# Kernel tuning notes

Hardware: AMD Instinct MI355X
Metric: run time of the kernel (lower is better)

## Reference

```python
import jax, jax.numpy as jnp
import numpy as np

B, S, D, H = 4, 2048, 256, 8
HD = D // H
SCALE = float(np.sqrt(HD))  # temperature = head_dim ** 0.5


def setup_inputs() -> dict:
    key = jax.random.key(0)
    ks = jax.random.split(key, 12)
    w = lambda k, shape: jax.random.normal(k, shape, dtype=jnp.float32) * 0.05
    x = jax.random.normal(ks[0], (B, S, D), dtype=jnp.float32)
    adj = jax.random.randint(ks[1], (B, S, S), 0, 2, dtype=jnp.int32)
    return {
        "x": x,
        "adj": adj,
        "w_qkv": w(ks[2], (3 * D, D)),
        "b_qkv": jnp.zeros((3 * D,), jnp.float32),
        "ln_g": jnp.ones((D,), jnp.float32),
        "ln_b": jnp.zeros((D,), jnp.float32),
        "w_fc": w(ks[3], (D, D)),
        "b_fc": jnp.zeros((D,), jnp.float32),
        "w_z": w(ks[4], (D, D)),
        "b_z": jnp.full((D,), -2.0, jnp.float32),  # init_bias fills w_z bias with -2
        "u_z": w(ks[5], (D, D)),
        "w_r": w(ks[6], (D, D)),
        "u_r": w(ks[7], (D, D)),
        "w_g": w(ks[8], (D, D)),
        "u_g": w(ks[9], (D, D)),
    }


def reference(x, adj, w_qkv, b_qkv, ln_g, ln_b, w_fc, b_fc,
              w_z, b_z, u_z, w_r, u_r, w_g, u_g):
    residual = x
    # LayerNorm (eps=1e-5, torch default)
    mu = jnp.mean(x, axis=-1, keepdims=True)
    var = jnp.var(x, axis=-1, keepdims=True)
    xn = (x - mu) / jnp.sqrt(var + 1e-5) * ln_g + ln_b
    # fused QKV projection -> (B*H, S, 3*HD), batch-major over (b, h)
    qkv = xn @ w_qkv.T + b_qkv                       # [B,S,3D]
    qkv = qkv.reshape(B, S, H, 3 * HD).transpose(0, 2, 1, 3).reshape(B * H, S, 3 * HD)
    q, k, v = jnp.split(qkv, 3, axis=-1)
    # masked scaled dot-product attention (full NxN scores, as in original)
    attn = jnp.einsum('nqd,nkd->nqk', q, k) / SCALE  # [B*H,S,S]
    adj_r = jnp.repeat(adj, H, axis=0)               # batch-major, matches attn layout
    attn = jnp.where(adj_r == 0, -jnp.inf, attn)
    attn = jax.nn.softmax(attn, axis=-1)
    out = jnp.einsum('nqk,nkd->nqd', attn, v)        # [B*H,S,HD]
    # Faithful replication of torch's view(n_head, batch, ...) applied to
    # batch-major data (an ordering quirk in the original module).
    out = out.reshape(H, B, S, HD).transpose(1, 2, 0, 3).reshape(B, S, D)
    y = jax.nn.relu(out @ w_fc.T + b_fc)
    # GRU gate: x=residual, y=attention branch
    z = jax.nn.sigmoid(y @ w_z.T + b_z + residual @ u_z.T)
    r = jax.nn.sigmoid(y @ w_r.T + residual @ u_r.T)
    h_hat = jnp.tanh(y @ w_g.T + (r * residual) @ u_g.T)
    return (1.0 - z) * residual + z * h_hat
```

## Files before the change

### kernel.cpp

```cpp
#include <hip/hip_runtime.h>
#include <hip/hip_bf16.h>
#include <math.h>

#define B_  4
#define S_  2048
#define D_  256
#define H_  8
#define HD_ 32
#define QSCALE 0.25504175929589786f

typedef short  bf16x8 __attribute__((ext_vector_type(8)));
typedef float  f32x4  __attribute__((ext_vector_type(4)));
typedef unsigned short ushort_t;
typedef unsigned int   uint_t;

__device__ __forceinline__ ushort_t f2b(float f) {
    union { float f; unsigned u; } v; v.f = f;
    unsigned r = (v.u + 0x7FFFu + ((v.u >> 16) & 1u)) >> 16;
    return (ushort_t)r;
}
__device__ __forceinline__ float b2f(ushort_t s) {
    return __uint_as_float((uint_t)s << 16);
}

__device__ __forceinline__ float wave_sum(float v) {
#pragma unroll
    for (int o = 32; o > 0; o >>= 1) v += __shfl_down(v, o, 64);
    return v;
}
__device__ __forceinline__ float block_sum256(float v, float* scr) {
    v = wave_sum(v);
    int lane = threadIdx.x & 63, wid = threadIdx.x >> 6;
    if (lane == 0) scr[wid] = v;
    __syncthreads();
    float r = scr[0] + scr[1] + scr[2] + scr[3];
    __syncthreads();
    return r;
}

#define WQ_SZ 196608
#define WS_SZ 65536
#define NB_ADJ 8192
#define NB_WC  2560
#define NB_LN  8192
__global__ __launch_bounds__(256)
void prep_kernel(const int* __restrict__ adj, uint_t* __restrict__ bits,
                 const float* __restrict__ w0, const float* __restrict__ w1,
                 const float* __restrict__ w2, const float* __restrict__ w3,
                 const float* __restrict__ w4, const float* __restrict__ w5,
                 const float* __restrict__ w6, const float* __restrict__ w7,
                 ushort_t* __restrict__ wout,
                 const float* __restrict__ x, const float* __restrict__ g,
                 const float* __restrict__ bb, ushort_t* __restrict__ xn_b) {
    __shared__ float scr[4];
    int blk = blockIdx.x, tid = threadIdx.x;
    if (blk < NB_ADJ) {
        int lane = tid & 63;
#pragma unroll
        for (int gp = 0; gp < 8; ++gp) {
            size_t i = ((size_t)blk * 8 + gp) * 256 + tid;
            unsigned long long m = __ballot(adj[i] != 0);
            size_t wbase = (((size_t)blk * 8 + gp) * 256 + (tid & ~63)) >> 5;
            if (lane == 0)  bits[wbase]     = (uint_t)m;
            if (lane == 32) bits[wbase + 1] = (uint_t)(m >> 32);
        }
    } else if (blk < NB_ADJ + NB_WC) {
        int idx = (blk - NB_ADJ) * 256 + tid;
        const float* src; int o;
        if (idx < WQ_SZ) { src = w0; o = idx; }
        else {
            int j = idx - WQ_SZ, seg = j >> 16; o = j & (WS_SZ - 1);
            src = (seg == 0) ? w1 : (seg == 1) ? w2 : (seg == 2) ? w3 :
                  (seg == 3) ? w4 : (seg == 4) ? w5 : (seg == 5) ? w6 : w7;
        }
        int j  = o & 7;
        int l  = (o >> 3) & 15;
        int qd = (o >> 7) & 3;
        int ks = (o >> 9) & 7;
        int ct = o >> 12;
        wout[idx] = f2b(src[(ct * 16 + l) * 256 + ks * 32 + qd * 8 + j]);
    } else {
        size_t base = (size_t)(blk - NB_ADJ - NB_WC) * D_;
        float v  = x[base + tid];
        float mu = block_sum256(v, scr) * (1.0f / D_);
        float d  = v - mu;
        float var = block_sum256(d * d, scr) * (1.0f / D_);
        float rstd = rsqrtf(var + 1e-5f);
        xn_b[base + tid] = f2b(d * rstd * g[tid] + bb[tid]);
    }
}

__global__ __launch_bounds__(256)
void gemm_qkv(const ushort_t* __restrict__ A, const ushort_t* __restrict__ Wf,
              const float* __restrict__ bias, ushort_t* __restrict__ outb,
              ushort_t* __restrict__ vT) {
    __shared__ ushort_t Sa[64][264];
    int tid = threadIdx.x;
    int wave = tid >> 6, lane = tid & 63, l = lane & 15, quad = lane >> 4;
    int wm = wave >> 1, wn = wave & 1;
    int m0 = blockIdx.y * 64, n0 = blockIdx.x * 64;
    {
        int row = tid >> 2, c0 = (tid & 3) * 64;
        const ushort_t* ap = A + (size_t)(m0 + row) * 256 + c0;
#pragma unroll
        for (int j = 0; j < 8; ++j)
            *(uint4*)&Sa[row][c0 + 8 * j] = ((const uint4*)ap)[j];
    }
    __syncthreads();

    bf16x8 af[2][8];
#pragma unroll
    for (int mt = 0; mt < 2; ++mt)
#pragma unroll
        for (int ks = 0; ks < 8; ++ks)
            af[mt][ks] = *(const bf16x8*)&Sa[wm * 32 + mt * 16 + l][ks * 32 + quad * 8];

    f32x4 acc[2][2];
#pragma unroll
    for (int i = 0; i < 2; ++i)
#pragma unroll
        for (int j = 0; j < 2; ++j) acc[i][j] = (f32x4){0.f, 0.f, 0.f, 0.f};

#pragma unroll
    for (int nt = 0; nt < 2; ++nt) {
        int ct = (n0 >> 4) + wn * 2 + nt;
        bf16x8 wfr[8];
#pragma unroll
        for (int ks = 0; ks < 8; ++ks)
            wfr[ks] = *(const bf16x8*)(Wf + (((size_t)ct * 8 + ks) * 64 + lane) * 8);
#pragma unroll
        for (int ks = 0; ks < 8; ++ks) {
            acc[0][nt] = __builtin_amdgcn_mfma_f32_16x16x32_bf16(af[0][ks], wfr[ks], acc[0][nt], 0, 0, 0);
            acc[1][nt] = __builtin_amdgcn_mfma_f32_16x16x32_bf16(af[1][ks], wfr[ks], acc[1][nt], 0, 0, 0);
        }
    }

    __syncthreads();
    ushort_t* So = &Sa[0][0];
#pragma unroll
    for (int nt = 0; nt < 2; ++nt) {
        int col = wn * 32 + nt * 16 + l;
        int gcol = n0 + col;
        float bv = bias[gcol];
        float qs = ((gcol % 96) < 32) ? QSCALE : 1.0f;
#pragma unroll
        for (int mt = 0; mt < 2; ++mt)
#pragma unroll
            for (int r = 0; r < 4; ++r) {
                int row = wm * 32 + mt * 16 + quad * 4 + r;
                So[row * 72 + col] = f2b((acc[mt][nt][r] + bv) * qs);
            }
    }
    __syncthreads();
    {
        int row = tid >> 2, seg = tid & 3;
        uint4 v0 = *(uint4*)&So[row * 72 + seg * 16];
        uint4 v1 = *(uint4*)&So[row * 72 + seg * 16 + 8];
        ushort_t* op = outb + (size_t)(m0 + row) * 768 + n0 + seg * 16;
        ((uint4*)op)[0] = v0;
        ((uint4*)op)[1] = v1;
    }

    int vs = n0 % 96;
    if (vs != 0) {
        int vloc = (vs == 64) ? 0 : 32;
        int h  = (n0 + vloc) / 96;
        int b  = m0 >> 11;
        int s0 = m0 & (S_ - 1);
        ushort_t* vstage = &Sa[0][0] + 8192;
        {
            int c = tid & 31, seg = tid >> 5;
            ushort_t tmp[8];
#pragma unroll
            for (int i = 0; i < 8; ++i)
                tmp[i] = So[(seg * 8 + i) * 72 + vloc + c];
            uint_t u[4];
#pragma unroll
            for (int i = 0; i < 4; ++i)
                u[i] = (uint_t)tmp[2 * i] | ((uint_t)tmp[2 * i + 1] << 16);
            *(uint4*)&vstage[c * 72 + seg * 8] = make_uint4(u[0], u[1], u[2], u[3]);
        }
        __syncthreads();
        {
            int d = tid >> 3, tseg = tid & 7;
            uint4 v = *(uint4*)&vstage[d * 72 + tseg * 8];
            *(uint4*)&vT[((size_t)(b * 8 + h) * 32 + d) * S_ + s0 + tseg * 8] = v;
        }
    }
}

__global__ __launch_bounds__(256)
void fused_gate(const ushort_t* __restrict__ attn_b, const float* __restrict__ xf,
                const ushort_t* __restrict__ wfc, const ushort_t* __restrict__ wz,
                const ushort_t* __restrict__ uz, const ushort_t* __restrict__ wr,
                const ushort_t* __restrict__ ur, const ushort_t* __restrict__ wg,
                const ushort_t* __restrict__ ug, const float* __restrict__ bfc,
                const float* __restrict__ bz, float* __restrict__ out) {
    __shared__ ushort_t Sa[16][264];
    __shared__ ushort_t Sx[16][264];
    __shared__ ushort_t Sy[16][264];
    __shared__ ushort_t St[16][264];
    int tid = threadIdx.x;
    int wave = tid >> 6, lane = tid & 63, l = lane & 15, quad = lane >> 4;
    int m0 = blockIdx.x * 16;
    int colbase = wave * 64;

    {
        int row = tid >> 4, c0 = (tid & 15) * 16;
        const ushort_t* ap = attn_b + (size_t)(m0 + row) * 256 + c0;
        uint4 a0 = ((const uint4*)ap)[0];
        uint4 a1 = ((const uint4*)ap)[1];
        *(uint4*)&Sa[row][c0] = a0;
        *(uint4*)&Sa[row][c0 + 8] = a1;
        const float4* xp = (const float4*)(xf + (size_t)(m0 + row) * 256 + c0);
        float4 f0 = xp[0], f1 = xp[1], f2_ = xp[2], f3 = xp[3];
        union { __hip_bfloat162 h[4]; uint4 u; } p0, p1;
        p0.h[0] = __float22bfloat162_rn(make_float2(f0.x, f0.y));
        p0.h[1] = __float22bfloat162_rn(make_float2(f0.z, f0.w));
        p0.h[2] = __float22bfloat162_rn(make_float2(f1.x, f1.y));
        p0.h[3] = __float22bfloat162_rn(make_float2(f1.z, f1.w));
        p1.h[0] = __float22bfloat162_rn(make_float2(f2_.x, f2_.y));
        p1.h[1] = __float22bfloat162_rn(make_float2(f2_.z, f2_.w));
        p1.h[2] = __float22bfloat162_rn(make_float2(f3.x, f3.y));
        p1.h[3] = __float22bfloat162_rn(make_float2(f3.z, f3.w));
        *(uint4*)&Sx[row][c0]     = p0.u;
        *(uint4*)&Sx[row][c0 + 8] = p1.u;
    }
    __syncthreads();

    {
        bf16x8 af[8];
#pragma unroll
        for (int ks = 0; ks < 8; ++ks)
            af[ks] = *(const bf16x8*)&Sa[l][ks * 32 + quad * 8];
        f32x4 ya[4];
#pragma unroll
        for (int nt = 0; nt < 4; ++nt) ya[nt] = (f32x4){0.f, 0.f, 0.f, 0.f};
#pragma unroll
        for (int nt = 0; nt < 4; ++nt) {
            size_t fb = ((size_t)(wave * 4 + nt) * 8) * 512 + lane * 8;
#pragma unroll
            for (int ks = 0; ks < 8; ++ks) {
                bf16x8 wfr = *(const bf16x8*)(wfc + fb + ks * 512);
                ya[nt] = __builtin_amdgcn_mfma_f32_16x16x32_bf16(af[ks], wfr, ya[nt], 0, 0, 0);
            }
        }
#pragma unroll
        for (int nt = 0; nt < 4; ++nt) {
            int col = colbase + nt * 16 + l;
            float bv = bfc[col];
#pragma unroll
            for (int r = 0; r < 4; ++r)
                Sy[quad * 4 + r][col] = f2b(fmaxf(ya[nt][r] + bv, 0.0f));
        }
    }
    __syncthreads();

    f32x4 az[4], ar[4], ag[4];
#pragma unroll
    for (int nt = 0; nt < 4; ++nt) {
        az[nt] = (f32x4){0.f, 0.f, 0.f, 0.f};
        ar[nt] = (f32x4){0.f, 0.f, 0.f, 0.f};
        ag[nt] = (f32x4){0.f, 0.f, 0.f, 0.f};
    }
#pragma unroll
    for (int nt = 0; nt < 4; ++nt) {
        size_t fb = ((size_t)(wave * 4 + nt) * 8) * 512 + lane * 8;
#pragma unroll
        for (int ks = 0; ks < 8; ++ks) {
            bf16x8 fy = *(const bf16x8*)&Sy[l][ks * 32 + quad * 8];
            bf16x8 fx = *(const bf16x8*)&Sx[l][ks * 32 + quad * 8];
            bf16x8 fz  = *(const bf16x8*)(wz + fb + ks * 512);
            bf16x8 fuz = *(const bf16x8*)(uz + fb + ks * 512);
            bf16x8 fr  = *(const bf16x8*)(wr + fb + ks * 512);
            bf16x8 fur = *(const bf16x8*)(ur + fb + ks * 512);
            bf16x8 fg  = *(const bf16x8*)(wg + fb + ks * 512);
            az[nt] = __builtin_amdgcn_mfma_f32_16x16x32_bf16(fy, fz,  az[nt], 0, 0, 0);
            az[nt] = __builtin_amdgcn_mfma_f32_16x16x32_bf16(fx, fuz, az[nt], 0, 0, 0);
            ar[nt] = __builtin_amdgcn_mfma_f32_16x16x32_bf16(fy, fr,  ar[nt], 0, 0, 0);
            ar[nt] = __builtin_amdgcn_mfma_f32_16x16x32_bf16(fx, fur, ar[nt], 0, 0, 0);
            ag[nt] = __builtin_amdgcn_mfma_f32_16x16x32_bf16(fy, fg,  ag[nt], 0, 0, 0);
        }
    }
#pragma unroll
    for (int nt = 0; nt < 4; ++nt) {
        int col = colbase + nt * 16 + l;
        float bzv = bz[col];
#pragma unroll
        for (int r = 0; r < 4; ++r) {
            int row = quad * 4 + r;
            az[nt][r] = 1.0f / (1.0f + __expf(-(az[nt][r] + bzv)));
            float rr  = 1.0f / (1.0f + __expf(-ar[nt][r]));
            St[row][col] = f2b(rr * b2f(Sx[row][col]));
        }
    }
    __syncthreads();

    f32x4 fcc[4];
#pragma unroll
    for (int nt = 0; nt < 4; ++nt) fcc[nt] = (f32x4){0.f, 0.f, 0.f, 0.f};
#pragma unroll
    for (int nt = 0; nt < 4; ++nt) {
        size_t fb = ((size_t)(wave * 4 + nt) * 8) * 512 + lane * 8;
#pragma unroll
        for (int ks = 0; ks < 8; ++ks) {
            bf16x8 ft = *(const bf16x8*)&St[l][ks * 32 + quad * 8];
            bf16x8 fu = *(const bf16x8*)(ug + fb + ks * 512);
            fcc[nt] = __builtin_amdgcn_mfma_f32_16x16x32_bf16(ft, fu, fcc[nt], 0, 0, 0);
        }
    }
#pragma unroll
    for (int nt = 0; nt < 4; ++nt) {
        int col = colbase + nt * 16 + l;
#pragma unroll
        for (int r = 0; r < 4; ++r) {
            int row = quad * 4 + r;
            float v = ag[nt][r] + fcc[nt][r];
            float e = __expf(2.0f * v);
            float h = 1.0f - 2.0f / (e + 1.0f);
            float zz = az[nt][r];
            size_t idx = (size_t)(m0 + row) * 256 + col;
            out[idx] = (1.0f - zz) * xf[idx] + zz * h;
        }
    }
}

__global__ __launch_bounds__(256)
void attn_kernel(const ushort_t* __restrict__ qkvb, const ushort_t* __restrict__ vT,
                 const uint_t* __restrict__ abits, ushort_t* __restrict__ attn_b) {
    __shared__ ushort_t Ks[2][64][40];
    __shared__ ushort_t Vt[2][32][72];
    __shared__ ushort_t Ps[64][72];

    int tid = threadIdx.x;
    int wave = tid >> 6, lane = tid & 63, l = lane & 15, quad = lane >> 4;

    int lid = blockIdx.y * 32 + blockIdx.x;
    int L   = (lid & 7) * 128 + (lid >> 3);
    int q0  = (L & 31) * 64;
    int n   = L >> 5;
    int b = n >> 3, h = n & 7;
    int bp = n & 3, hp = n >> 2;

    const ushort_t* base = qkvb + (size_t)b * S_ * 768 + h * 96;
    int myq = wave * 16 + l;
    int qsh = quad * 4;

    bf16x8 qf = *(const bf16x8*)(base + (size_t)(q0 + myq) * 768 + quad * 8);

    bf16x8 ones;
#pragma unroll
    for (int i = 0; i < 8; ++i) ones[i] = (short)0x3F80;

    f32x4 oacc[2], aones;
    oacc[0] = (f32x4){0.f, 0.f, 0.f, 0.f};
    oacc[1] = (f32x4){0.f, 0.f, 0.f, 0.f};
    aones   = (f32x4){0.f, 0.f, 0.f, 0.f};

    int skey = tid >> 2, spart = tid & 3;
    int kcol = (spart * 8) ^ (((skey >> 3) & 1) << 3);
    int vd = tid >> 3, vk = (tid & 7) * 8;
    const ushort_t* vptr = vT + ((size_t)n * 32 + vd) * S_ + vk;
    const uint_t* aptr = abits + ((size_t)b * S_ + q0 + myq) * 64;

    uint2 aw = *(const uint2*)(aptr);
    {
        uint4 k0v = *(const uint4*)(base + (size_t)skey * 768 + 32 + spart * 8);
        uint4 v0v = *(const uint4*)(vptr);
        *(uint4*)&Ks[0][skey][kcol] = k0v;
        *(uint4*)&Vt[0][vd][vk] = v0v;
    }
    uint4 kv = *(const uint4*)(base + (size_t)(64 + skey) * 768 + 32 + spart * 8);
    uint4 vv = *(const uint4*)(vptr + 64);
    __syncthreads();

    for (int k0 = 0; k0 < S_; k0 += 64) {
        int cur = (k0 >> 6) & 1;
        bool more = (k0 + 64 < S_);
        uint2 awn;
        if (more) {
            *(uint4*)&Ks[cur ^ 1][skey][kcol] = kv;
            *(uint4*)&Vt[cur ^ 1][vd][vk] = vv;
            awn = *(const uint2*)(aptr + ((k0 + 64) >> 5));
            if (k0 + 128 < S_) {
                kv = *(const uint4*)(base + (size_t)(k0 + 128 + skey) * 768 + 32 + spart * 8);
                vv = *(const uint4*)(vptr + k0 + 128);
            }
        }
        uint_t aw0 = aw.x, aw1 = aw.y;

#pragma unroll
        for (int t4 = 0; t4 < 4; ++t4) {
            bf16x8 kf = *(const bf16x8*)&Ks[cur][t4 * 16 + l][(quad * 8) ^ ((l >> 3) << 3)];
            f32x4 z = (f32x4){0.f, 0.f, 0.f, 0.f};
            f32x4 sc = __builtin_amdgcn_mfma_f32_16x16x32_bf16(kf, qf, z, 0, 0, 0);
            uint_t w = (t4 & 2) ? aw1 : aw0;
            uint_t idx = (w >> ((t4 & 1) * 16 + qsh)) & 15u;
            union { __hip_bfloat162 b2[2]; uint2 u2; } pk;
            pk.b2[0] = __float22bfloat162_rn(make_float2(exp2f(sc[0]), exp2f(sc[1])));
            pk.b2[1] = __float22bfloat162_rn(make_float2(exp2f(sc[2]), exp2f(sc[3])));
            pk.u2.x &= ((idx & 1u) ? 0xFFFFu : 0u) | ((idx & 2u) ? 0xFFFF0000u : 0u);
            pk.u2.y &= ((idx & 4u) ? 0xFFFFu : 0u) | ((idx & 8u) ? 0xFFFF0000u : 0u);
            *(uint2*)&Ps[myq][t4 * 16 + qsh] = pk.u2;
        }

        __builtin_amdgcn_s_setprio(1);
#pragma unroll
        for (int ks = 0; ks < 2; ++ks) {
            bf16x8 pf = *(const bf16x8*)&Ps[myq][ks * 32 + quad * 8];
            aones = __builtin_amdgcn_mfma_f32_16x16x32_bf16(ones, pf, aones, 0, 0, 0);
#pragma unroll
            for (int mt = 0; mt < 2; ++mt) {
                bf16x8 vf = *(const bf16x8*)&Vt[cur][mt * 16 + l][ks * 32 + quad * 8];
                oacc[mt] = __builtin_amdgcn_mfma_f32_16x16x32_bf16(vf, pf, oacc[mt], 0, 0, 0);
            }
        }
        __builtin_amdgcn_s_setprio(0);

        if (more) aw = awn;
        __syncthreads();
    }

    float linv = 1.0f / aones[0];

    ushort_t* Ost = &Ks[0][0][0];
#pragma unroll
    for (int mt = 0; mt < 2; ++mt)
#pragma unroll
        for (int r = 0; r < 4; ++r)
            Ost[myq * 40 + mt * 16 + quad * 4 + r] = f2b(oacc[mt][r] * linv);
    __syncthreads();
    {
        int q = tid >> 2, part = tid & 3;
        uint4 v = *(uint4*)&Ost[q * 40 + part * 8];
        *(uint4*)&attn_b[((size_t)(bp * S_ + q0 + q)) * 256 + hp * 32 + part * 8] = v;
    }
}

extern "C" void kernel_launch(void* const* d_in, const int* in_sizes, int n_in,
                              void* d_out, int out_size, void* d_ws, size_t ws_size,
                              hipStream_t stream) {
    const float* x     = (const float*)d_in[0];
    const int*   adj   = (const int*)d_in[1];
    const float* w_qkv = (const float*)d_in[2];
    const float* b_qkv = (const float*)d_in[3];
    const float* ln_g  = (const float*)d_in[4];
    const float* ln_b  = (const float*)d_in[5];
    const float* w_fc  = (const float*)d_in[6];
    const float* b_fc  = (const float*)d_in[7];
    const float* w_z   = (const float*)d_in[8];
    const float* b_z   = (const float*)d_in[9];
    const float* u_z   = (const float*)d_in[10];
    const float* w_r   = (const float*)d_in[11];
    const float* u_r   = (const float*)d_in[12];
    const float* w_g   = (const float*)d_in[13];
    const float* u_g   = (const float*)d_in[14];
    float* out = (float*)d_out;

    const size_t TOK  = (size_t)B_ * S_;
    const size_t TOKD = TOK * D_;
    ushort_t* xn_b   = (ushort_t*)d_ws;
    ushort_t* qkv_b  = xn_b + TOKD;
    ushort_t* attn_b = qkv_b + TOK * 768;
    ushort_t* wb     = attn_b + TOKD;
    uint_t*   bits   = (uint_t*)(wb + WQ_SZ + 7 * WS_SZ);
    ushort_t* vTb    = (ushort_t*)(bits + (size_t)B_ * S_ * S_ / 32);

    ushort_t* wq_b  = wb;
    ushort_t* wfc_b = wb + WQ_SZ;
    ushort_t* wz_b  = wfc_b + WS_SZ;
    ushort_t* uz_b  = wz_b + WS_SZ;
    ushort_t* wr_b  = uz_b + WS_SZ;
    ushort_t* ur_b  = wr_b + WS_SZ;
    ushort_t* wg_b  = ur_b + WS_SZ;
    ushort_t* ug_b  = wg_b + WS_SZ;

    prep_kernel<<<NB_ADJ + NB_WC + NB_LN, 256, 0, stream>>>(
        adj, bits, w_qkv, w_fc, w_z, u_z, w_r, u_r, w_g, u_g, wb,
        x, ln_g, ln_b, xn_b);

    gemm_qkv<<<dim3(12, 128), 256, 0, stream>>>(xn_b, wq_b, b_qkv, qkv_b, vTb);

    attn_kernel<<<dim3(S_ / 64, B_ * H_), 256, 0, stream>>>(qkv_b, vTb, bits, attn_b);

    fused_gate<<<512, 256, 0, stream>>>(
        attn_b, x, wfc_b, wz_b, uz_b, wr_b, ur_b, wg_b, ug_b, b_fc, b_z, out);
}
```

Measured before the change: 241.8 us.

## Switch attention to 32x32x16 MFMA with register-resident P and 128-query tiles

Rewrites the attention kernel to use 32x32x16 bf16 MFMA instructions with 32 queries per wave and 128 queries per block. The scores accumulator layout now matches the B/A operand layout needed for the PV product, so the probability tile stays in registers instead of round-tripping through shared memory. K rows are permuted when stored to LDS to line up with that layout. This halves the number of blocks, doubles K/V reuse per load, and removes the Ps buffer, at the cost of more registers per thread and fewer blocks in flight.

```diff
diff --git a/kernel.cpp b/kernel.cpp
--- a/kernel.cpp
+++ b/kernel.cpp
@@ -11,6 +11,7 @@
 
 typedef short  bf16x8 __attribute__((ext_vector_type(8)));
 typedef float  f32x4  __attribute__((ext_vector_type(4)));
+typedef float  f32x16 __attribute__((ext_vector_type(16)));
 typedef unsigned short ushort_t;
 typedef unsigned int   uint_t;
 
@@ -21,6 +22,12 @@
 }
 __device__ __forceinline__ float b2f(ushort_t s) {
     return __uint_as_float((uint_t)s << 16);
+}
+__device__ __forceinline__ f32x16 zero16() {
+    f32x16 z;
+#pragma unroll
+    for (int i = 0; i < 16; ++i) z[i] = 0.f;
+    return z;
 }
 
 __device__ __forceinline__ float wave_sum(float v) {
@@ -330,56 +337,58 @@
                  const uint_t* __restrict__ abits, ushort_t* __restrict__ attn_b) {
     __shared__ ushort_t Ks[2][64][40];
     __shared__ ushort_t Vt[2][32][72];
-    __shared__ ushort_t Ps[64][72];
 
     int tid = threadIdx.x;
-    int wave = tid >> 6, lane = tid & 63, l = lane & 15, quad = lane >> 4;
-
-    int lid = blockIdx.y * 32 + blockIdx.x;
-    int L   = (lid & 7) * 128 + (lid >> 3);
-    int q0  = (L & 31) * 64;
-    int n   = L >> 5;
+    int wave = tid >> 6, lane = tid & 63;
+    int lane5 = lane & 31, hi = lane >> 5;
+    int hsh8 = hi * 8;
+
+    int lid = blockIdx.y * 16 + blockIdx.x;
+    int L   = (lid & 7) * 64 + (lid >> 3);
+    int q0  = (L & 15) * 128;
+    int n   = L >> 4;
     int b = n >> 3, h = n & 7;
     int bp = n & 3, hp = n >> 2;
 
     const ushort_t* base = qkvb + (size_t)b * S_ * 768 + h * 96;
-    int myq = wave * 16 + l;
-    int qsh = quad * 4;
-
-    bf16x8 qf = *(const bf16x8*)(base + (size_t)(q0 + myq) * 768 + quad * 8);
+    int qbase = wave * 32;
+    int myq = q0 + qbase + lane5;
+
+    bf16x8 qf1 = *(const bf16x8*)(base + (size_t)myq * 768 + hsh8);
+    bf16x8 qf2 = *(const bf16x8*)(base + (size_t)myq * 768 + 16 + hsh8);
 
     bf16x8 ones;
 #pragma unroll
     for (int i = 0; i < 8; ++i) ones[i] = (short)0x3F80;
 
-    f32x4 oacc[2], aones;
-    oacc[0] = (f32x4){0.f, 0.f, 0.f, 0.f};
-    oacc[1] = (f32x4){0.f, 0.f, 0.f, 0.f};
-    aones   = (f32x4){0.f, 0.f, 0.f, 0.f};
+    f32x16 oacc = zero16(), aones = zero16();
 
     int skey = tid >> 2, spart = tid & 3;
-    int kcol = (spart * 8) ^ (((skey >> 3) & 1) << 3);
+    int prow = (skey & ~12) | ((skey & 4) << 1) | ((skey & 8) >> 1);
+    int kcol = (spart * 8) ^ (((prow >> 3) & 1) << 3);
     int vd = tid >> 3, vk = (tid & 7) * 8;
     const ushort_t* vptr = vT + ((size_t)n * 32 + vd) * S_ + vk;
-    const uint_t* aptr = abits + ((size_t)b * S_ + q0 + myq) * 64;
-
-    uint2 aw = *(const uint2*)(aptr);
+    const uint_t* aptr = abits + ((size_t)b * S_ + myq) * 64;
+
+    uint2 aw = *(const uint2*)aptr;
     {
         uint4 k0v = *(const uint4*)(base + (size_t)skey * 768 + 32 + spart * 8);
         uint4 v0v = *(const uint4*)(vptr);
-        *(uint4*)&Ks[0][skey][kcol] = k0v;
+        *(uint4*)&Ks[0][prow][kcol] = k0v;
         *(uint4*)&Vt[0][vd][vk] = v0v;
     }
     uint4 kv = *(const uint4*)(base + (size_t)(64 + skey) * 768 + 32 + spart * 8);
     uint4 vv = *(const uint4*)(vptr + 64);
     __syncthreads();
+
+    int b3 = (lane >> 3) & 1;
 
     for (int k0 = 0; k0 < S_; k0 += 64) {
         int cur = (k0 >> 6) & 1;
         bool more = (k0 + 64 < S_);
         uint2 awn;
         if (more) {
-            *(uint4*)&Ks[cur ^ 1][skey][kcol] = kv;
+            *(uint4*)&Ks[cur ^ 1][prow][kcol] = kv;
             *(uint4*)&Vt[cur ^ 1][vd][vk] = vv;
             awn = *(const uint2*)(aptr + ((k0 + 64) >> 5));
             if (k0 + 128 < S_) {
@@ -387,53 +396,61 @@
                 vv = *(const uint4*)(vptr + k0 + 128);
             }
         }
-        uint_t aw0 = aw.x, aw1 = aw.y;
-
-#pragma unroll
-        for (int t4 = 0; t4 < 4; ++t4) {
-            bf16x8 kf = *(const bf16x8*)&Ks[cur][t4 * 16 + l][(quad * 8) ^ ((l >> 3) << 3)];
-            f32x4 z = (f32x4){0.f, 0.f, 0.f, 0.f};
-            f32x4 sc = __builtin_amdgcn_mfma_f32_16x16x32_bf16(kf, qf, z, 0, 0, 0);
-            uint_t w = (t4 & 2) ? aw1 : aw0;
-            uint_t idx = (w >> ((t4 & 1) * 16 + qsh)) & 15u;
-            union { __hip_bfloat162 b2[2]; uint2 u2; } pk;
-            pk.b2[0] = __float22bfloat162_rn(make_float2(exp2f(sc[0]), exp2f(sc[1])));
-            pk.b2[1] = __float22bfloat162_rn(make_float2(exp2f(sc[2]), exp2f(sc[3])));
-            pk.u2.x &= ((idx & 1u) ? 0xFFFFu : 0u) | ((idx & 2u) ? 0xFFFF0000u : 0u);
-            pk.u2.y &= ((idx & 4u) ? 0xFFFFu : 0u) | ((idx & 8u) ? 0xFFFF0000u : 0u);
-            *(uint2*)&Ps[myq][t4 * 16 + qsh] = pk.u2;
-        }
-
-        __builtin_amdgcn_s_setprio(1);
-#pragma unroll
-        for (int ks = 0; ks < 2; ++ks) {
-            bf16x8 pf = *(const bf16x8*)&Ps[myq][ks * 32 + quad * 8];
-            aones = __builtin_amdgcn_mfma_f32_16x16x32_bf16(ones, pf, aones, 0, 0, 0);
-#pragma unroll
-            for (int mt = 0; mt < 2; ++mt) {
-                bf16x8 vf = *(const bf16x8*)&Vt[cur][mt * 16 + l][ks * 32 + quad * 8];
-                oacc[mt] = __builtin_amdgcn_mfma_f32_16x16x32_bf16(vf, pf, oacc[mt], 0, 0, 0);
+        uint_t awx = aw.x, awy = aw.y;
+
+#pragma unroll
+        for (int kb2 = 0; kb2 < 2; ++kb2) {
+            const int kb = kb2 * 32;
+            bf16x8 kf1 = *(const bf16x8*)&Ks[cur][kb + lane5][(hi ^ b3) * 8];
+            bf16x8 kf2 = *(const bf16x8*)&Ks[cur][kb + lane5][((2 + hi) ^ b3) * 8];
+            f32x16 sc = zero16();
+            sc = __builtin_amdgcn_mfma_f32_32x32x16_bf16(kf1, qf1, sc, 0, 0, 0);
+            sc = __builtin_amdgcn_mfma_f32_32x32x16_bf16(kf2, qf2, sc, 0, 0, 0);
+
+            uint_t wsub = (kb2 ? awy : awx) >> hsh8;
+            union { uint_t u[8]; bf16x8 v[2]; } pp;
+#pragma unroll
+            for (int i = 0; i < 8; ++i) {
+                const int c = 2 * i + ((i >> 2) * 8);
+                float e0 = exp2f(sc[2 * i]);
+                float e1 = exp2f(sc[2 * i + 1]);
+                uint_t m0 = (uint_t)((int)(wsub << (31 - c)) >> 31);
+                uint_t m1 = (uint_t)((int)(wsub << (30 - c)) >> 31);
+                e0 = __uint_as_float(__float_as_uint(e0) & m0);
+                e1 = __uint_as_float(__float_as_uint(e1) & m1);
+                union { __hip_bfloat162 b2; uint_t u; } p;
+                p.b2 = __float22bfloat162_rn(make_float2(e0, e1));
+                pp.u[i] = p.u;
             }
-        }
-        __builtin_amdgcn_s_setprio(0);
+
+            bf16x8 vb1 = *(const bf16x8*)&Vt[cur][lane5][kb + hsh8];
+            bf16x8 vb2 = *(const bf16x8*)&Vt[cur][lane5][kb + 16 + hsh8];
+
+            __builtin_amdgcn_s_setprio(1);
+            oacc  = __builtin_amdgcn_mfma_f32_32x32x16_bf16(pp.v[0], vb1,  oacc,  0, 0, 0);
+            aones = __builtin_amdgcn_mfma_f32_32x32x16_bf16(pp.v[0], ones, aones, 0, 0, 0);
+            oacc  = __builtin_amdgcn_mfma_f32_32x32x16_bf16(pp.v[1], vb2,  oacc,  0, 0, 0);
+            aones = __builtin_amdgcn_mfma_f32_32x32x16_bf16(pp.v[1], ones, aones, 0, 0, 0);
+            __builtin_amdgcn_s_setprio(0);
+        }
 
         if (more) aw = awn;
         __syncthreads();
     }
 
-    float linv = 1.0f / aones[0];
-
     ushort_t* Ost = &Ks[0][0][0];
 #pragma unroll
-    for (int mt = 0; mt < 2; ++mt)
-#pragma unroll
-        for (int r = 0; r < 4; ++r)
-            Ost[myq * 40 + mt * 16 + quad * 4 + r] = f2b(oacc[mt][r] * linv);
-    __syncthreads();
-    {
-        int q = tid >> 2, part = tid & 3;
-        uint4 v = *(uint4*)&Ost[q * 40 + part * 8];
-        *(uint4*)&attn_b[((size_t)(bp * S_ + q0 + q)) * 256 + hp * 32 + part * 8] = v;
+    for (int r = 0; r < 16; ++r) {
+        int qr = (r & 3) + 8 * (r >> 2) + 4 * hi;
+        Ost[(qbase + qr) * 40 + lane5] = f2b(oacc[r] / aones[r]);
+    }
+    __syncthreads();
+#pragma unroll
+    for (int bt = 0; bt < 2; ++bt) {
+        int row = (tid >> 2) + bt * 64;
+        int part = tid & 3;
+        uint4 v = *(uint4*)&Ost[row * 40 + part * 8];
+        *(uint4*)&attn_b[((size_t)(bp * S_ + q0 + row)) * 256 + hp * 32 + part * 8] = v;
     }
 }
 
@@ -481,7 +498,7 @@
 
     gemm_qkv<<<dim3(12, 128), 256, 0, stream>>>(xn_b, wq_b, b_qkv, qkv_b, vTb);
 
-    attn_kernel<<<dim3(S_ / 64, B_ * H_), 256, 0, stream>>>(qkv_b, vTb, bits, attn_b);
+    attn_kernel<<<dim3(S_ / 128, B_ * H_), 256, 0, stream>>>(qkv_b, vTb, bits, attn_b);
 
     fused_gate<<<512, 256, 0, stream>>>(
         attn_b, x, wfc_b, wz_b, uz_b, wr_b, ur_b, wg_b, ug_b, b_fc, b_z, out);
```

Measured after the change: 235.9 us. -2.5%, faster.
